# Optimization experiments

Measured on AMD Instinct MI355X. Metric: run time of the kernel, lower is better.

## Reference

```python
import jax, jax.numpy as jnp
import numpy as np

DT = 0.001          # time step
P = 2               # geomloss p -> cost = ||x-y||^2 / 2, eps = blur**p
BLUR = 0.01
SCALING = 0.5       # eps annealing ratio per step is SCALING**P
SPARSE = 1          # sparse_sampling
N_STEPS = 24        # fixed annealing+refinement iteration count (jit-static)


def setup_inputs() -> dict:
    key = jax.random.key(0)
    k1, k2 = jax.random.split(key)
    B, S, NT, NR = 2, 4, 256, 64
    syn_data = jax.random.normal(k1, (B, S, NT, NR), jnp.float32)
    obs_data = jax.random.normal(k2, (B, S, NT, NR), jnp.float32)
    return {"syn_data": syn_data, "obs_data": obs_data}


def _softmin(eps, C, h):
    # h: [m] = log-weights + potential/eps ; C: [n, m]
    return -eps * jax.nn.logsumexp(h[None, :] - C / eps, axis=1)


def _pairwise_cost(a, b):
    # geomloss p=2 cost: squared euclidean distance / 2
    return 0.5 * jnp.sum((a[:, None, :] - b[None, :, :]) ** 2, axis=-1)


def _sinkhorn_divergence(x, y):
    # x, y: [n, 2] point clouds with uniform weights 1/n.
    # Debiased Sinkhorn divergence S = OT_eps(x,y) - 0.5 OT(x,x) - 0.5 OT(y,y)
    # computed via log-domain iterations with epsilon annealing from
    # diameter**p down to blur**p (ratio scaling**p), as in geomloss.
    n = x.shape[0]
    la = jnp.full((n,), -np.log(n), x.dtype)  # log uniform weights
    Cxy = _pairwise_cost(x, y)
    Cyx = Cxy.T
    Cxx = _pairwise_cost(x, x)
    Cyy = _pairwise_cost(y, y)

    xy = jnp.concatenate([x, y], axis=0)
    diameter = jnp.max(jnp.max(xy, axis=0) - jnp.min(xy, axis=0))
    eps0 = diameter ** P
    eps_min = jnp.asarray(BLUR ** P, x.dtype)
    ratio = SCALING ** P
    eps_list = jnp.maximum(eps0 * ratio ** jnp.arange(N_STEPS, dtype=x.dtype), eps_min)

    zeros = jnp.zeros((n,), x.dtype)

    def step(carry, eps):
        f, g, px, py = carry
        f_new = _softmin(eps, Cxy, la + g / eps)
        g_new = _softmin(eps, Cyx, la + f / eps)
        # symmetric (debiasing) potentials use damped fixed-point updates
        px_new = 0.5 * (px + _softmin(eps, Cxx, la + px / eps))
        py_new = 0.5 * (py + _softmin(eps, Cyy, la + py / eps))
        return (f_new, g_new, px_new, py_new), None

    (f, g, px, py), _ = jax.lax.scan(step, (zeros, zeros, zeros, zeros), eps_list)
    w = jnp.exp(la)  # uniform 1/n
    return jnp.sum(w * (f - px)) + jnp.sum(w * (g - py))


def reference(syn_data, obs_data):
    B, S, NT, NR = syn_data.shape
    # trace mask: drop receiver only if BOTH obs and syn traces are all-zero
    mask1 = jnp.sum(jnp.abs(obs_data), axis=2) == 0  # [B,S,NR]
    mask2 = jnp.sum(jnp.abs(syn_data), axis=2) == 0
    mask = ~(mask1 & mask2)

    t = jnp.arange(NT, dtype=syn_data.dtype)[::SPARSE] * DT  # [NTs]
    obs_tr = jnp.swapaxes(obs_data[:, :, ::SPARSE, :], 2, 3)  # [B,S,NR,NTs]
    syn_tr = jnp.swapaxes(syn_data[:, :, ::SPARSE, :], 2, 3)
    tb = jnp.broadcast_to(t, obs_tr.shape)
    obs_pts = jnp.stack([tb, obs_tr], axis=-1)  # [B,S,NR,NTs,2]
    syn_pts = jnp.stack([tb, syn_tr], axis=-1)

    nts = obs_pts.shape[3]
    flat_obs = obs_pts.reshape(B * S * NR, nts, 2)
    flat_syn = syn_pts.reshape(B * S * NR, nts, 2)
    div = jax.vmap(_sinkhorn_divergence)(flat_obs, flat_syn)  # [B*S*NR]
    div = div.reshape(B, S, NR)
    return jnp.sum(jnp.where(mask, div, jnp.zeros_like(div)), axis=(1, 2))  # [B]
```

## Files before the change

### kernel.cpp

```cpp
#include <hip/hip_runtime.h>


constexpr int   N       = 256;
constexpr int   NPROB   = 512;
constexpr int   NRDIM   = 64;
constexpr float DT_F    = 0.001f;
constexpr float EPS_MIN = 1e-4f;
constexpr int   NSTEPS  = 24;
constexpr float LOG2E   = 1.4426950408889634f;
constexpr float LN2     = 0.6931471805599453f;
constexpr int   NT      = 1024;
constexpr int   CPQ     = 64;

extern "C" __global__ void __launch_bounds__(NT, 8)
sinkhorn_div_kernel(const float* __restrict__ syn,
                    const float* __restrict__ obs,
                    float* __restrict__ divs)
{
    const int p   = blockIdx.x;
    const int r   = p & (NRDIM - 1);
    const int bs  = p >> 6;
    const int tid = threadIdx.x;
    const int row = tid & (N - 1);
    const int q   = tid >> 8;

    __shared__ float4 ya[N];
    __shared__ float4 xa[N];
    __shared__ float4 msh[NT];
    __shared__ float4 ssh[NT];
    __shared__ float  redA[64];

    const size_t base = (size_t)bs * N * NRDIM + r;
    const float xi = obs[base + (size_t)row * NRDIM];
    const float yi = syn[base + (size_t)row * NRDIM];

    float hi = fmaxf(xi, yi), lo = fminf(xi, yi);
    float ax = fabsf(xi),     ay = fabsf(yi);
    #pragma unroll
    for (int off = 32; off > 0; off >>= 1) {
        hi  = fmaxf(hi, __shfl_down(hi, off, 64));
        lo  = fminf(lo, __shfl_down(lo, off, 64));
        ax += __shfl_down(ax, off, 64);
        ay += __shfl_down(ay, off, 64);
    }
    const int wave = tid >> 6;
    if ((tid & 63) == 0) {
        redA[wave * 4 + 0] = hi;  redA[wave * 4 + 1] = lo;
        redA[wave * 4 + 2] = ax;  redA[wave * 4 + 3] = ay;
    }
    __syncthreads();
    float vmax = -3.4e38f, vmin = 3.4e38f, sax = 0.0f, say = 0.0f;
    #pragma unroll
    for (int w = 0; w < 16; ++w) {
        vmax = fmaxf(vmax, redA[w * 4 + 0]);
        vmin = fminf(vmin, redA[w * 4 + 1]);
        sax += redA[w * 4 + 2];
        say += redA[w * 4 + 3];
    }

    const float tspread  = 255.0f * DT_F;
    const float diameter = fmaxf(tspread, vmax - vmin);
    float eps_raw = diameter * diameter;

    const float ti    = (float)row * DT_F;
    const float selfx = 0.5f * (ti * ti + xi * xi);
    const float selfy = 0.5f * (ti * ti + yi * yi);

    float f = 0.0f, g = 0.0f, px = 0.0f, py = 0.0f;

    const int j0 = q * CPQ;

    for (int step = 0; step < NSTEPS; ++step) {
        const float eps = fmaxf(eps_raw, EPS_MIN);
        const float inv = LOG2E / eps;

        if (q == 0) {
            const float la2 = -8.0f;
            const float Hxy = fmaf(g  - selfy, inv, la2);
            const float Hyy = fmaf(py - selfy, inv, la2);
            const float Hyx = fmaf(f  - selfx, inv, la2);
            const float Hxx = fmaf(px - selfx, inv, la2);
            ya[row] = make_float4(Hxy, Hyy, yi * inv, 0.0f);
            xa[row] = make_float4(Hyx, Hxx, xi * inv, 0.0f);
        }
        __syncthreads();

        const float a = ti * DT_F * inv;

        {
            float m0 = -1e9f, m1 = -1e9f, s0 = 0.0f, s1 = 0.0f;
            float rr = a * (float)j0;
            for (int cc = 0; cc < CPQ; cc += 8) {
                float b[8], c[8];
                #pragma unroll
                for (int k = 0; k < 8; ++k) {
                    const float4 yA = ya[j0 + cc + k];
                    b[k] = fmaf(xi, yA.z, yA.x + rr);
                    c[k] = fmaf(yi, yA.z, yA.y + rr);
                    rr += a;
                }
                const float mc0 = fmaxf(fmaxf(fmaxf(b[0], b[1]), fmaxf(b[2], b[3])),
                                        fmaxf(fmaxf(b[4], b[5]), fmaxf(b[6], b[7])));
                const float mc1 = fmaxf(fmaxf(fmaxf(c[0], c[1]), fmaxf(c[2], c[3])),
                                        fmaxf(fmaxf(c[4], c[5]), fmaxf(c[6], c[7])));
                const float M0 = fmaxf(m0, ceilf(mc0));
                const float M1 = fmaxf(m1, ceilf(mc1));
                const float t0 =
                    (__builtin_amdgcn_exp2f(b[0] - M0) + __builtin_amdgcn_exp2f(b[1] - M0)) +
                    (__builtin_amdgcn_exp2f(b[2] - M0) + __builtin_amdgcn_exp2f(b[3] - M0)) +
                   ((__builtin_amdgcn_exp2f(b[4] - M0) + __builtin_amdgcn_exp2f(b[5] - M0)) +
                    (__builtin_amdgcn_exp2f(b[6] - M0) + __builtin_amdgcn_exp2f(b[7] - M0)));
                const float t1 =
                    (__builtin_amdgcn_exp2f(c[0] - M1) + __builtin_amdgcn_exp2f(c[1] - M1)) +
                    (__builtin_amdgcn_exp2f(c[2] - M1) + __builtin_amdgcn_exp2f(c[3] - M1)) +
                   ((__builtin_amdgcn_exp2f(c[4] - M1) + __builtin_amdgcn_exp2f(c[5] - M1)) +
                    (__builtin_amdgcn_exp2f(c[6] - M1) + __builtin_amdgcn_exp2f(c[7] - M1)));
                s0 = ldexpf(s0, (int)(m0 - M0)) + t0;  m0 = M0;
                s1 = ldexpf(s1, (int)(m1 - M1)) + t1;  m1 = M1;
            }
            msh[tid] = make_float4(m0, m1, s0, s1);
        }

        {
            float m2 = -1e9f, m3 = -1e9f, s2 = 0.0f, s3 = 0.0f;
            float rr = a * (float)j0;
            for (int cc = 0; cc < CPQ; cc += 8) {
                float b[8], c[8];
                #pragma unroll
                for (int k = 0; k < 8; ++k) {
                    const float4 xA = xa[j0 + cc + k];
                    b[k] = fmaf(yi, xA.z, xA.x + rr);
                    c[k] = fmaf(xi, xA.z, xA.y + rr);
                    rr += a;
                }
                const float mc2 = fmaxf(fmaxf(fmaxf(b[0], b[1]), fmaxf(b[2], b[3])),
                                        fmaxf(fmaxf(b[4], b[5]), fmaxf(b[6], b[7])));
                const float mc3 = fmaxf(fmaxf(fmaxf(c[0], c[1]), fmaxf(c[2], c[3])),
                                        fmaxf(fmaxf(c[4], c[5]), fmaxf(c[6], c[7])));
                const float M2 = fmaxf(m2, ceilf(mc2));
                const float M3 = fmaxf(m3, ceilf(mc3));
                const float t2 =
                    (__builtin_amdgcn_exp2f(b[0] - M2) + __builtin_amdgcn_exp2f(b[1] - M2)) +
                    (__builtin_amdgcn_exp2f(b[2] - M2) + __builtin_amdgcn_exp2f(b[3] - M2)) +
                   ((__builtin_amdgcn_exp2f(b[4] - M2) + __builtin_amdgcn_exp2f(b[5] - M2)) +
                    (__builtin_amdgcn_exp2f(b[6] - M2) + __builtin_amdgcn_exp2f(b[7] - M2)));
                const float t3 =
                    (__builtin_amdgcn_exp2f(c[0] - M3) + __builtin_amdgcn_exp2f(c[1] - M3)) +
                    (__builtin_amdgcn_exp2f(c[2] - M3) + __builtin_amdgcn_exp2f(c[3] - M3)) +
                   ((__builtin_amdgcn_exp2f(c[4] - M3) + __builtin_amdgcn_exp2f(c[5] - M3)) +
                    (__builtin_amdgcn_exp2f(c[6] - M3) + __builtin_amdgcn_exp2f(c[7] - M3)));
                s2 = ldexpf(s2, (int)(m2 - M2)) + t2;  m2 = M2;
                s3 = ldexpf(s3, (int)(m3 - M3)) + t3;  m3 = M3;
            }
            ssh[tid] = make_float4(m2, m3, s2, s3);
        }
        __syncthreads();

        const float4 A0 = msh[row];
        const float4 A1 = msh[row + 256];
        const float4 A2 = msh[row + 512];
        const float4 A3 = msh[row + 768];
        const float4 B0 = ssh[row];
        const float4 B1 = ssh[row + 256];
        const float4 B2 = ssh[row + 512];
        const float4 B3 = ssh[row + 768];

        const float Mxy = fmaxf(fmaxf(A0.x, A1.x), fmaxf(A2.x, A3.x));
        const float Myy = fmaxf(fmaxf(A0.y, A1.y), fmaxf(A2.y, A3.y));
        const float Myx = fmaxf(fmaxf(B0.x, B1.x), fmaxf(B2.x, B3.x));
        const float Mxx = fmaxf(fmaxf(B0.y, B1.y), fmaxf(B2.y, B3.y));

        const float Sxy = (ldexpf(A0.z, (int)(A0.x - Mxy)) + ldexpf(A1.z, (int)(A1.x - Mxy)))
                        + (ldexpf(A2.z, (int)(A2.x - Mxy)) + ldexpf(A3.z, (int)(A3.x - Mxy)));
        const float Syy = (ldexpf(A0.w, (int)(A0.y - Myy)) + ldexpf(A1.w, (int)(A1.y - Myy)))
                        + (ldexpf(A2.w, (int)(A2.y - Myy)) + ldexpf(A3.w, (int)(A3.y - Myy)));
        const float Syx = (ldexpf(B0.z, (int)(B0.x - Myx)) + ldexpf(B1.z, (int)(B1.x - Myx)))
                        + (ldexpf(B2.z, (int)(B2.x - Myx)) + ldexpf(B3.z, (int)(B3.x - Myx)));
        const float Sxx = (ldexpf(B0.w, (int)(B0.y - Mxx)) + ldexpf(B1.w, (int)(B1.y - Mxx)))
                        + (ldexpf(B2.w, (int)(B2.y - Mxx)) + ldexpf(B3.w, (int)(B3.y - Mxx)));

        const float el2 = eps * LN2;
        const float fn  = selfx - el2 * (Mxy + __builtin_amdgcn_logf(Sxy));
        const float gn  = selfy - el2 * (Myx + __builtin_amdgcn_logf(Syx));
        const float pxn = 0.5f * (px + (selfx - el2 * (Mxx + __builtin_amdgcn_logf(Sxx))));
        const float pyn = 0.5f * (py + (selfy - el2 * (Myy + __builtin_amdgcn_logf(Syy))));
        f = fn; g = gn; px = pxn; py = pyn;

        eps_raw *= 0.25f;
    }

    float contrib = (f - px) + (g - py);
    #pragma unroll
    for (int off = 32; off > 0; off >>= 1)
        contrib += __shfl_down(contrib, off, 64);
    __syncthreads();
    if ((tid & 63) == 0) redA[wave] = contrib;
    __syncthreads();
    if (tid == 0) {
        float total = 0.0f;
        #pragma unroll
        for (int w = 0; w < 16; ++w) total += redA[w];
        total *= (1.0f / (float)(4 * N));
        const bool masked_out = (sax == 0.0f) && (say == 0.0f);
        divs[p] = masked_out ? 0.0f : total;
    }
}

extern "C" __global__ void __launch_bounds__(256)
reduce_out_kernel(const float* __restrict__ divs, float* __restrict__ out)
{
    const int b   = blockIdx.x;
    const int tid = threadIdx.x;
    __shared__ float red[4];
    float v = divs[b * 256 + tid];
    #pragma unroll
    for (int off = 32; off > 0; off >>= 1)
        v += __shfl_down(v, off, 64);
    if ((tid & 63) == 0) red[tid >> 6] = v;
    __syncthreads();
    if (tid == 0) out[b] = red[0] + red[1] + red[2] + red[3];
}

extern "C" void kernel_launch(void* const* d_in, const int* in_sizes, int n_in,
                              void* d_out, int out_size, void* d_ws, size_t ws_size,
                              hipStream_t stream) {
    const float* syn = (const float*)d_in[0];
    const float* obs = (const float*)d_in[1];
    float* divs = (float*)d_ws;

    sinkhorn_div_kernel<<<NPROB, NT, 0, stream>>>(syn, obs, divs);
    reduce_out_kernel<<<2, 256, 0, stream>>>(divs, (float*)d_out);
}
```

Measured before the change: 656.0 us.

## Repack shared H arrays and vectorize LDS loads; trim redundant epilogue work

The padded float4 per-column shared arrays become float2 H pairs plus separate raw-value arrays. The inner loop now loads 8 columns with six 128-bit LDS reads instead of eight, and multiplies the raw value by a per-thread xi/inv or yi/inv factor instead of a stored y*inv. Writing the H arrays is split between two thread quarters, and only quarters 0 and 1 run the final logsumexp merge, each computing only the potentials it needs. Only quarter 0 contributes to the final sum, with the normalisation changed from 1/(4N) to 1/N to match. The aim is less LDS traffic and less duplicated epilogue arithmetic, at the cost of extra divergent branches.

After: 697.3 us. 6.3% more time.

```diff
diff --git a/kernel.cpp b/kernel.cpp
--- a/kernel.cpp
+++ b/kernel.cpp
@@ -24,8 +24,10 @@
     const int row = tid & (N - 1);
     const int q   = tid >> 8;
 
-    __shared__ float4 ya[N];
-    __shared__ float4 xa[N];
+    __shared__ float2 ya2[N];
+    __shared__ float2 xa2[N];
+    __shared__ float  yraw[N];
+    __shared__ float  xraw[N];
     __shared__ float4 msh[NT];
     __shared__ float4 ssh[NT];
     __shared__ float  redA[64];
@@ -33,6 +35,8 @@
     const size_t base = (size_t)bs * N * NRDIM + r;
     const float xi = obs[base + (size_t)row * NRDIM];
     const float yi = syn[base + (size_t)row * NRDIM];
+
+    if (q == 0) { yraw[row] = yi; xraw[row] = xi; }
 
     float hi = fmaxf(xi, yi), lo = fminf(xi, yi);
     float ax = fabsf(xi),     ay = fabsf(yi);
@@ -65,39 +69,50 @@
     const float ti    = (float)row * DT_F;
     const float selfx = 0.5f * (ti * ti + xi * xi);
     const float selfy = 0.5f * (ti * ti + yi * yi);
+    const float la2   = -8.0f;
 
     float f = 0.0f, g = 0.0f, px = 0.0f, py = 0.0f;
 
     const int j0 = q * CPQ;
 
     for (int step = 0; step < NSTEPS; ++step) {
-        const float eps = fmaxf(eps_raw, EPS_MIN);
-        const float inv = LOG2E / eps;
+        const float eps  = fmaxf(eps_raw, EPS_MIN);
+        const float inv  = LOG2E / eps;
+        const float xinv = xi * inv;
+        const float yinv = yi * inv;
 
         if (q == 0) {
-            const float la2 = -8.0f;
-            const float Hxy = fmaf(g  - selfy, inv, la2);
-            const float Hyy = fmaf(py - selfy, inv, la2);
-            const float Hyx = fmaf(f  - selfx, inv, la2);
-            const float Hxx = fmaf(px - selfx, inv, la2);
-            ya[row] = make_float4(Hxy, Hyy, yi * inv, 0.0f);
-            xa[row] = make_float4(Hyx, Hxx, xi * inv, 0.0f);
+            ya2[row] = make_float2(fmaf(g  - selfy, inv, la2),
+                                   fmaf(py - selfy, inv, la2));
+        } else if (q == 1) {
+            xa2[row] = make_float2(fmaf(f  - selfx, inv, la2),
+                                   fmaf(px - selfx, inv, la2));
         }
         __syncthreads();
 
-        const float a = ti * DT_F * inv;
+        const float a  = ti * DT_F * inv;
+        const float a8 = 8.0f * a;
 
         {
             float m0 = -1e9f, m1 = -1e9f, s0 = 0.0f, s1 = 0.0f;
-            float rr = a * (float)j0;
+            float rr0 = a * (float)j0;
             for (int cc = 0; cc < CPQ; cc += 8) {
+                const int j = j0 + cc;
+                const float4 hA = *(const float4*)&ya2[j + 0];
+                const float4 hB = *(const float4*)&ya2[j + 2];
+                const float4 hC = *(const float4*)&ya2[j + 4];
+                const float4 hD = *(const float4*)&ya2[j + 6];
+                const float4 rA = *(const float4*)&yraw[j + 0];
+                const float4 rB = *(const float4*)&yraw[j + 4];
+                const float hx[8] = {hA.x, hA.z, hB.x, hB.z, hC.x, hC.z, hD.x, hD.z};
+                const float hy[8] = {hA.y, hA.w, hB.y, hB.w, hC.y, hC.w, hD.y, hD.w};
+                const float rw[8] = {rA.x, rA.y, rA.z, rA.w, rB.x, rB.y, rB.z, rB.w};
                 float b[8], c[8];
                 #pragma unroll
                 for (int k = 0; k < 8; ++k) {
-                    const float4 yA = ya[j0 + cc + k];
-                    b[k] = fmaf(xi, yA.z, yA.x + rr);
-                    c[k] = fmaf(yi, yA.z, yA.y + rr);
-                    rr += a;
+                    const float rk = fmaf((float)k, a, rr0);
+                    b[k] = fmaf(xinv, rw[k], hx[k] + rk);
+                    c[k] = fmaf(yinv, rw[k], hy[k] + rk);
                 }
                 const float mc0 = fmaxf(fmaxf(fmaxf(b[0], b[1]), fmaxf(b[2], b[3])),
                                         fmaxf(fmaxf(b[4], b[5]), fmaxf(b[6], b[7])));
@@ -117,21 +132,31 @@
                     (__builtin_amdgcn_exp2f(c[6] - M1) + __builtin_amdgcn_exp2f(c[7] - M1)));
                 s0 = ldexpf(s0, (int)(m0 - M0)) + t0;  m0 = M0;
                 s1 = ldexpf(s1, (int)(m1 - M1)) + t1;  m1 = M1;
+                rr0 += a8;
             }
             msh[tid] = make_float4(m0, m1, s0, s1);
         }
 
         {
             float m2 = -1e9f, m3 = -1e9f, s2 = 0.0f, s3 = 0.0f;
-            float rr = a * (float)j0;
+            float rr0 = a * (float)j0;
             for (int cc = 0; cc < CPQ; cc += 8) {
+                const int j = j0 + cc;
+                const float4 hA = *(const float4*)&xa2[j + 0];
+                const float4 hB = *(const float4*)&xa2[j + 2];
+                const float4 hC = *(const float4*)&xa2[j + 4];
+                const float4 hD = *(const float4*)&xa2[j + 6];
+                const float4 rA = *(const float4*)&xraw[j + 0];
+                const float4 rB = *(const float4*)&xraw[j + 4];
+                const float hx[8] = {hA.x, hA.z, hB.x, hB.z, hC.x, hC.z, hD.x, hD.z};
+                const float hy[8] = {hA.y, hA.w, hB.y, hB.w, hC.y, hC.w, hD.y, hD.w};
+                const float rw[8] = {rA.x, rA.y, rA.z, rA.w, rB.x, rB.y, rB.z, rB.w};
                 float b[8], c[8];
                 #pragma unroll
                 for (int k = 0; k < 8; ++k) {
-                    const float4 xA = xa[j0 + cc + k];
-                    b[k] = fmaf(yi, xA.z, xA.x + rr);
-                    c[k] = fmaf(xi, xA.z, xA.y + rr);
-                    rr += a;
+                    const float rk = fmaf((float)k, a, rr0);
+                    b[k] = fmaf(yinv, rw[k], hx[k] + rk);
+                    c[k] = fmaf(xinv, rw[k], hy[k] + rk);
                 }
                 const float mc2 = fmaxf(fmaxf(fmaxf(b[0], b[1]), fmaxf(b[2], b[3])),
                                         fmaxf(fmaxf(b[4], b[5]), fmaxf(b[6], b[7])));
@@ -151,45 +176,50 @@
                     (__builtin_amdgcn_exp2f(c[6] - M3) + __builtin_amdgcn_exp2f(c[7] - M3)));
                 s2 = ldexpf(s2, (int)(m2 - M2)) + t2;  m2 = M2;
                 s3 = ldexpf(s3, (int)(m3 - M3)) + t3;  m3 = M3;
+                rr0 += a8;
             }
             ssh[tid] = make_float4(m2, m3, s2, s3);
         }
         __syncthreads();
 
-        const float4 A0 = msh[row];
-        const float4 A1 = msh[row + 256];
-        const float4 A2 = msh[row + 512];
-        const float4 A3 = msh[row + 768];
-        const float4 B0 = ssh[row];
-        const float4 B1 = ssh[row + 256];
-        const float4 B2 = ssh[row + 512];
-        const float4 B3 = ssh[row + 768];
-
-        const float Mxy = fmaxf(fmaxf(A0.x, A1.x), fmaxf(A2.x, A3.x));
-        const float Myy = fmaxf(fmaxf(A0.y, A1.y), fmaxf(A2.y, A3.y));
-        const float Myx = fmaxf(fmaxf(B0.x, B1.x), fmaxf(B2.x, B3.x));
-        const float Mxx = fmaxf(fmaxf(B0.y, B1.y), fmaxf(B2.y, B3.y));
-
-        const float Sxy = (ldexpf(A0.z, (int)(A0.x - Mxy)) + ldexpf(A1.z, (int)(A1.x - Mxy)))
-                        + (ldexpf(A2.z, (int)(A2.x - Mxy)) + ldexpf(A3.z, (int)(A3.x - Mxy)));
-        const float Syy = (ldexpf(A0.w, (int)(A0.y - Myy)) + ldexpf(A1.w, (int)(A1.y - Myy)))
-                        + (ldexpf(A2.w, (int)(A2.y - Myy)) + ldexpf(A3.w, (int)(A3.y - Myy)));
-        const float Syx = (ldexpf(B0.z, (int)(B0.x - Myx)) + ldexpf(B1.z, (int)(B1.x - Myx)))
-                        + (ldexpf(B2.z, (int)(B2.x - Myx)) + ldexpf(B3.z, (int)(B3.x - Myx)));
-        const float Sxx = (ldexpf(B0.w, (int)(B0.y - Mxx)) + ldexpf(B1.w, (int)(B1.y - Mxx)))
-                        + (ldexpf(B2.w, (int)(B2.y - Mxx)) + ldexpf(B3.w, (int)(B3.y - Mxx)));
-
-        const float el2 = eps * LN2;
-        const float fn  = selfx - el2 * (Mxy + __builtin_amdgcn_logf(Sxy));
-        const float gn  = selfy - el2 * (Myx + __builtin_amdgcn_logf(Syx));
-        const float pxn = 0.5f * (px + (selfx - el2 * (Mxx + __builtin_amdgcn_logf(Sxx))));
-        const float pyn = 0.5f * (py + (selfy - el2 * (Myy + __builtin_amdgcn_logf(Syy))));
-        f = fn; g = gn; px = pxn; py = pyn;
+        if (q <= 1) {
+            const float4 A0 = msh[row];
+            const float4 A1 = msh[row + 256];
+            const float4 A2 = msh[row + 512];
+            const float4 A3 = msh[row + 768];
+            const float4 B0 = ssh[row];
+            const float4 B1 = ssh[row + 256];
+            const float4 B2 = ssh[row + 512];
+            const float4 B3 = ssh[row + 768];
+            const float el2 = eps * LN2;
+
+            const float Mxy = fmaxf(fmaxf(A0.x, A1.x), fmaxf(A2.x, A3.x));
+            const float Sxy = (ldexpf(A0.z, (int)(A0.x - Mxy)) + ldexpf(A1.z, (int)(A1.x - Mxy)))
+                            + (ldexpf(A2.z, (int)(A2.x - Mxy)) + ldexpf(A3.z, (int)(A3.x - Mxy)));
+            const float Mxx = fmaxf(fmaxf(B0.y, B1.y), fmaxf(B2.y, B3.y));
+            const float Sxx = (ldexpf(B0.w, (int)(B0.y - Mxx)) + ldexpf(B1.w, (int)(B1.y - Mxx)))
+                            + (ldexpf(B2.w, (int)(B2.y - Mxx)) + ldexpf(B3.w, (int)(B3.y - Mxx)));
+
+            const float fn  = selfx - el2 * (Mxy + __builtin_amdgcn_logf(Sxy));
+            const float pxn = 0.5f * (px + (selfx - el2 * (Mxx + __builtin_amdgcn_logf(Sxx))));
+
+            if (q == 0) {
+                const float Myx = fmaxf(fmaxf(B0.x, B1.x), fmaxf(B2.x, B3.x));
+                const float Syx = (ldexpf(B0.z, (int)(B0.x - Myx)) + ldexpf(B1.z, (int)(B1.x - Myx)))
+                                + (ldexpf(B2.z, (int)(B2.x - Myx)) + ldexpf(B3.z, (int)(B3.x - Myx)));
+                const float Myy = fmaxf(fmaxf(A0.y, A1.y), fmaxf(A2.y, A3.y));
+                const float Syy = (ldexpf(A0.w, (int)(A0.y - Myy)) + ldexpf(A1.w, (int)(A1.y - Myy)))
+                                + (ldexpf(A2.w, (int)(A2.y - Myy)) + ldexpf(A3.w, (int)(A3.y - Myy)));
+                g  = selfy - el2 * (Myx + __builtin_amdgcn_logf(Syx));
+                py = 0.5f * (py + (selfy - el2 * (Myy + __builtin_amdgcn_logf(Syy))));
+            }
+            f = fn; px = pxn;
+        }
 
         eps_raw *= 0.25f;
     }
 
-    float contrib = (f - px) + (g - py);
+    float contrib = (q == 0) ? ((f - px) + (g - py)) : 0.0f;
     #pragma unroll
     for (int off = 32; off > 0; off >>= 1)
         contrib += __shfl_down(contrib, off, 64);
@@ -200,7 +230,7 @@
         float total = 0.0f;
         #pragma unroll
         for (int w = 0; w < 16; ++w) total += redA[w];
-        total *= (1.0f / (float)(4 * N));
+        total *= (1.0f / (float)N);
         const bool masked_out = (sax == 0.0f) && (say == 0.0f);
         divs[p] = masked_out ? 0.0f : total;
     }
```
